# Kernel tuning notes

Measured on AMD Instinct MI355X. Metric: run time of the kernel, lower is better.

## Reference

```python
import jax, jax.numpy as jnp
import numpy as np

K = 3
KK = K * K
EPS = 1e-5


def conv2d(x, w, b, pad):
    y = jax.lax.conv_general_dilated(x, w, (1, 1), [(pad, pad), (pad, pad)],
                                     dimension_numbers=("NCHW", "OIHW", "NCHW"))
    return y + b[None, :, None, None]


def bn(x, g, b, m, v):
    inv = g / jnp.sqrt(v + EPS)
    return x * inv[None, :, None, None] + (b - m * inv)[None, :, None, None]


def deform_sample(x, dy, dx):
    # x: [B,C,H,W]; dy,dx: [B,KK,H,W] -> sampled [B,C,KK,H,W] (bilinear, zeros outside)
    B, C, H, W = x.shape
    k = jnp.arange(K, dtype=x.dtype) - 1.0  # pad=1, dilation=1, stride=1
    ky = jnp.repeat(k, K)  # [KK] row offsets
    kx = jnp.tile(k, K)    # [KK] col offsets
    hh = jnp.arange(H, dtype=x.dtype)
    ww = jnp.arange(W, dtype=x.dtype)
    py = hh[None, :, None] + ky[:, None, None] + dy  # [B,KK,H,W]
    px = ww[None, None, :] + kx[:, None, None] + dx

    def sample_one(img, py, px):
        y0f = jnp.floor(py); x0f = jnp.floor(px)
        wy = py - y0f; wx = px - x0f
        y0 = y0f.astype(jnp.int32); x0 = x0f.astype(jnp.int32)

        def gather(yi, xi, w):
            valid = (yi >= 0) & (yi < H) & (xi >= 0) & (xi < W)
            yc = jnp.clip(yi, 0, H - 1); xc = jnp.clip(xi, 0, W - 1)
            v = img[:, yc, xc]  # [C,KK,H,W]
            return v * (w * valid)[None]

        return (gather(y0, x0, (1 - wy) * (1 - wx)) +
                gather(y0, x0 + 1, (1 - wy) * wx) +
                gather(y0 + 1, x0, wy * (1 - wx)) +
                gather(y0 + 1, x0 + 1, wy * wx))

    return jax.vmap(sample_one)(x, py, px)


def setup_inputs() -> dict:
    key = jax.random.key(0)
    ks = jax.random.split(key, 16)
    B, C, H, W = 8, 256, 64, 64
    d = {
        "feature": jax.random.normal(ks[0], (B, C, H, W), jnp.float32),
        "p1_w": jax.random.normal(ks[1], (C, C, 1, 1), jnp.float32) * 0.05,
        "p1_b": jax.random.normal(ks[2], (C,), jnp.float32) * 0.05,
        "bn1_g": jax.random.normal(ks[3], (C,), jnp.float32) * 0.1 + 1.0,
        "bn1_b": jax.random.normal(ks[4], (C,), jnp.float32) * 0.05,
        "bn1_m": jax.random.normal(ks[5], (C,), jnp.float32) * 0.05,
        "bn1_v": jax.random.uniform(ks[6], (C,), jnp.float32) + 0.5,
        "off_w": jax.random.normal(ks[7], (3 * KK, 2 * C, K, K), jnp.float32) * 0.01,
        "off_b": jax.random.normal(ks[8], (3 * KK,), jnp.float32) * 0.01,
        "dcn_w": jax.random.normal(ks[9], (C, C, K, K), jnp.float32) * 0.05,
        "dcn_b": jax.random.normal(ks[10], (C,), jnp.float32) * 0.05,
        "bn2_g": jax.random.normal(ks[11], (C,), jnp.float32) * 0.1 + 1.0,
        "bn2_b": jax.random.normal(ks[12], (C,), jnp.float32) * 0.05,
        "bn2_m": jax.random.normal(ks[13], (C,), jnp.float32) * 0.05,
        "bn2_v": jax.random.uniform(ks[14], (C,), jnp.float32) + 0.5,
    }
    return d


def reference(feature, p1_w, p1_b, bn1_g, bn1_b, bn1_m, bn1_v,
              off_w, off_b, dcn_w, dcn_b, bn2_g, bn2_b, bn2_m, bn2_v):
    flipped = feature[..., ::-1]                      # flip last (W) axis
    proj = bn(conv2d(feature, p1_w, p1_b, 0), bn1_g, bn1_b, bn1_m, bn1_v)
    # DCNv2: offsets/mask from concat(flipped, proj)
    concat = jnp.concatenate([flipped, proj], axis=1)
    off = conv2d(concat, off_w, off_b, 1)             # [B,27,H,W]
    dy = off[:, :KK]
    dx = off[:, KK:2 * KK]
    mask = jax.nn.sigmoid(off[:, 2 * KK:])            # [B,KK,H,W]
    sampled = deform_sample(flipped, dy, dx)          # [B,C,KK,H,W]
    O = dcn_w.shape[0]
    y = jnp.einsum("bckhw,ock->bohw", sampled * mask[:, None], dcn_w.reshape(O, -1, KK))
    y = y + dcn_b[None, :, None, None]
    y = bn(y, bn2_g, bn2_b, bn2_m, bn2_v)
    return jax.nn.relu(proj + y)
```

## Files before the change

### kernel.cpp

```cpp
#include <hip/hip_runtime.h>
#include <hip/hip_bf16.h>
#include <math.h>

typedef __attribute__((ext_vector_type(8))) short short8;
typedef __attribute__((ext_vector_type(4))) short short4v;
typedef __attribute__((ext_vector_type(4))) float f32x4;
typedef __attribute__((ext_vector_type(2))) float f32x2;

__device__ __forceinline__ float bs2f(short s){
    union { unsigned u; float f; } x; x.u = ((unsigned)(unsigned short)s) << 16; return x.f;
}
__device__ __forceinline__ short f2bs(float f){
    union { float f; unsigned u; } x; x.f = f;
    unsigned r = x.u + 0x7fff + ((x.u >> 16) & 1);
    return (short)(r >> 16);
}
__device__ __forceinline__ f32x2 up2(unsigned u){
    union { unsigned u; float f; } lo, hi;
    lo.u = u << 16; hi.u = u & 0xffff0000u;
    f32x2 r; r.x = lo.f; r.y = hi.f; return r;
}
__device__ __forceinline__ unsigned pk2rn(float lo, float hi){
    __hip_bfloat162 h = __float22bfloat162_rn(make_float2(lo, hi));
    union { __hip_bfloat162 h; unsigned u; } cv; cv.h = h; return cv.u;
}
__device__ __forceinline__ void gl2lds16(const void* g, void* l){
    __builtin_amdgcn_global_load_lds(
        (const __attribute__((address_space(1))) void*)g,
        (__attribute__((address_space(3))) void*)l, 16, 0, 0);
}
__device__ __forceinline__ void hard_barrier(){
    __builtin_amdgcn_sched_barrier(0);
    __builtin_amdgcn_s_barrier();
    __builtin_amdgcn_sched_barrier(0);
}
__device__ __forceinline__ void lds_barrier(){
    __builtin_amdgcn_sched_barrier(0);
    asm volatile("s_waitcnt lgkmcnt(0)" ::: "memory");
    __builtin_amdgcn_s_barrier();
    __builtin_amdgcn_sched_barrier(0);
}

#define XPB ((size_t)66*66*512)


__global__ void k_prep(const float* __restrict__ p1_w, const float* __restrict__ p1_b,
                       const float* __restrict__ bn1_g, const float* __restrict__ bn1_b,
                       const float* __restrict__ bn1_m, const float* __restrict__ bn1_v,
                       const float* __restrict__ off_w,
                       const float* __restrict__ dcn_w, const float* __restrict__ dcn_b,
                       const float* __restrict__ bn2_g, const float* __restrict__ bn2_b,
                       const float* __restrict__ bn2_m, const float* __restrict__ bn2_v,
                       short* __restrict__ p1_wb, short* __restrict__ Wofrag,
                       short* __restrict__ Wfrag,
                       float* __restrict__ bias1f, float* __restrict__ inv2f,
                       float* __restrict__ bias2f, unsigned* __restrict__ XpadU)
{
    int blk = blockIdx.x, t = threadIdx.x;
    if (blk == 0) {
        float inv1 = bn1_g[t] / sqrtf(bn1_v[t] + 1e-5f);
        bias1f[t] = p1_b[t] * inv1 + bn1_b[t] - bn1_m[t] * inv1;
        float inv2 = bn2_g[t] / sqrtf(bn2_v[t] + 1e-5f);
        inv2f[t] = inv2;
        bias2f[t] = dcn_b[t] * inv2 + bn2_b[t] - bn2_m[t] * inv2;
    } else if (blk <= 256) {
        int o = blk - 1;
        float inv1 = bn1_g[o] / sqrtf(bn1_v[o] + 1e-5f);
        p1_wb[o*256 + t] = f2bs(p1_w[o*256 + t] * inv1);
    } else if (blk <= 512) {
        int o = blk - 257;
        const float* src = dcn_w + (size_t)o*2304;
        uint4* dst = (uint4*)Wfrag;
        int strip = o >> 4, lnn = o & 15;
        #pragma unroll
        for (int r = 0; r < 2; ++r) {
            int j = r*256 + t;
            if (j < 288) {
                int tap = j >> 5, c0 = (j & 31) * 8;
                union { short s[8]; uint4 u; } v;
                #pragma unroll
                for (int e = 0; e < 8; ++e)
                    v.s[e] = f2bs(src[(c0 + e)*9 + tap]);
                dst[(size_t)((j >> 2)*16 + strip)*64 + (j & 3)*16 + lnn] = v.u;
            }
        }
    } else if (blk <= 584) {
        int gidx = (blk - 513)*256 + t;
        int kc = gidx >> 7;
        int rem = gidx & 127;
        int strip = rem >> 6, lane2 = rem & 63;
        int ln2 = lane2 & 15, q2 = lane2 >> 4;
        int row = strip*16 + ln2;
        union { short s[8]; uint4 u; } v;
        #pragma unroll
        for (int e = 0; e < 8; ++e) {
            int k = kc*32 + q2*8 + e;
            int tap = k >> 9, ci = k & 511;
            v.s[e] = (row < 27) ? f2bs(off_w[(size_t)row*4608 + ci*9 + tap]) : (short)0;
        }
        ((uint4*)Wofrag)[gidx] = v.u;
    } else {
        int hb = blk - 585;
        int b = hb / 260, i = hb % 260;
        int y, x;
        if (i < 66)       { y = 0;  x = i; }
        else if (i < 132) { y = 65; x = i - 66; }
        else { int j = i - 132; y = 1 + (j >> 1); x = (j & 1) * 65; }
        XpadU[((size_t)(b*66 + y)*66 + x)*256 + t] = 0u;
    }
}

__global__ __launch_bounds__(512, 2) void k_fproj(
    const float* __restrict__ feature, short* Xpad,
    const short* __restrict__ p1_wb, const float* __restrict__ bias1f)
{
    __shared__ __align__(16) unsigned char sh_u[16640];
    __shared__ __align__(16) short Bt[8][2048];
    float (*tile)[65] = (float(*)[65])sh_u;
    short* Ash = (short*)sh_u;
    int bid = blockIdx.x;
    int b = bid & 7, h = bid >> 3;
    int t = threadIdx.x;
    int lane = t & 63, w = t >> 6;
    int lw = t & 63, li = t >> 6;
    int ln = lane & 15, q = lane >> 4;
    int r16 = lane >> 2;
    int sq  = (lane & 3) ^ ((lane >> 3) & 3);
    int rq  = (q ^ ((ln >> 1) & 3)) * 8;
    size_t rowbase = (size_t)(b*66 + h + 1)*66;

    for (int cg = 0; cg < 4; ++cg) {
        int c0 = cg * 64;
        #pragma unroll
        for (int j = 0; j < 8; ++j) {
            int cl = j*8 + li;
            tile[cl][63 - lw] = feature[((b*256 + c0 + cl)*64 + h)*64 + lw];
        }
        __syncthreads();
        #pragma unroll
        for (int j = 0; j < 8; ++j) {
            int x = j*8 + li;
            short s  = f2bs(tile[lw][x]);
            Xpad[(rowbase + x + 1)*512 + c0 + lw] = s;
            short sB = f2bs(tile[lw][63 - x]);
            int c = c0 + lw;
            int kt = c >> 5, kk = c & 31, p = kk >> 3, e = kk & 7;
            Bt[kt][x*32 + ((p ^ ((x >> 1) & 3)) << 3) + e] = sB;
        }
        __syncthreads();
    }

    f32x4 acc[2][4] = {};
    for (int kt = 0; kt < 8; ++kt) {
        int kcol = kt*32 + sq*8;
        #pragma unroll
        for (int i = 0; i < 2; ++i) {
            int row = w*32 + i*16 + r16;
            gl2lds16(p1_wb + (size_t)row*256 + kcol, Ash + (w*32 + i*16)*32);
        }
        __syncthreads();
        short8 af[2], bfr[4];
        #pragma unroll
        for (int i = 0; i < 2; ++i)
            af[i] = *(const short8*)&Ash[(w*32 + i*16 + ln)*32 + rq];
        #pragma unroll
        for (int j = 0; j < 4; ++j)
            bfr[j] = *(const short8*)&Bt[kt][(j*16 + ln)*32 + rq];
        #pragma unroll
        for (int i = 0; i < 2; ++i)
            #pragma unroll
            for (int j = 0; j < 4; ++j)
                acc[i][j] = __builtin_amdgcn_mfma_f32_16x16x32_bf16(af[i], bfr[j], acc[i][j], 0, 0, 0);
        __syncthreads();
    }
    #pragma unroll
    for (int i = 0; i < 2; ++i) {
        int ob = w*32 + i*16 + q*4;
        #pragma unroll
        for (int j = 0; j < 4; ++j) {
            int x = j*16 + ln;
            size_t xb = (rowbase + x + 1)*512 + 256 + ob;
            short4v st;
            st.x = f2bs(acc[i][j][0] + bias1f[ob]);
            st.y = f2bs(acc[i][j][1] + bias1f[ob+1]);
            st.z = f2bs(acc[i][j][2] + bias1f[ob+2]);
            st.w = f2bs(acc[i][j][3] + bias1f[ob+3]);
            *(short4v*)&Xpad[xb] = st;
        }
    }
}

#define ALOAD4(kn_, A_)                                                   \
    A_##0 = Wf4[(size_t)(((kn_)*2+0)*16 + tw0)*64 + lane];                \
    A_##1 = Wf4[(size_t)(((kn_)*2+0)*16 + tw1)*64 + lane];                \
    A_##2 = Wf4[(size_t)(((kn_)*2+1)*16 + tw0)*64 + lane];                \
    A_##3 = Wf4[(size_t)(((kn_)*2+1)*16 + tw1)*64 + lane];

#define MMPHASE(A_)                                                       \
    {                                                                     \
        short8 af00 = *(short8*)&A_##0, af01 = *(short8*)&A_##1;          \
        short8 af10 = *(short8*)&A_##2, af11 = *(short8*)&A_##3;          \
        short8 bfr;                                                       \
        _Pragma("unroll")                                                 \
        for (int jj = 0; jj < 4; ++jj) {                                  \
            bfr = *(const short8*)&Bsh[0][(jj*16 + ln)*32 + rq];          \
            acc[0][jj] = __builtin_amdgcn_mfma_f32_16x16x32_bf16(af00, bfr, acc[0][jj], 0, 0, 0); \
            acc[1][jj] = __builtin_amdgcn_mfma_f32_16x16x32_bf16(af01, bfr, acc[1][jj], 0, 0, 0); \
        }                                                                 \
        _Pragma("unroll")                                                 \
        for (int jj = 0; jj < 4; ++jj) {                                  \
            bfr = *(const short8*)&Bsh[1][(jj*16 + ln)*32 + rq];          \
            acc[0][jj] = __builtin_amdgcn_mfma_f32_16x16x32_bf16(af10, bfr, acc[0][jj], 0, 0, 0); \
            acc[1][jj] = __builtin_amdgcn_mfma_f32_16x16x32_bf16(af11, bfr, acc[1][jj], 0, 0, 0); \
        }                                                                 \
    }

#define WINX(kc2_, AC_, AN_, UC_, VN_)                                    \
    {                                                                     \
        int kn_ = (kc2_) < 35 ? (kc2_) + 1 : 35;                          \
        ALOAD4(kn_, AN_);                                                 \
        GATHER(kn_, VN_);                                                 \
        __builtin_amdgcn_sched_barrier(0);                                \
        BLEND(UC_, (kc2_) >> 2);                                          \
        lds_barrier();                                                    \
        MMPHASE(AC_);                                                     \
        hard_barrier();                                                   \
    }

__global__ __launch_bounds__(512, 4) void k_gemm(
    const short* __restrict__ Xpad,
    const short* __restrict__ Wfrag,
    const uint4* __restrict__ Wof4,
    const float* __restrict__ off_b,
    const float* __restrict__ inv2f, const float* __restrict__ bias2f,
    float* __restrict__ out)
{
    __shared__ __align__(16) unsigned char shU[32768];
    __shared__ float red[27][65];
    short (*BshO)[2048] = (short(*)[2048])shU;
    short (*Bsh)[2048]  = (short(*)[2048])shU;
    unsigned* c_pk = (unsigned*)(shU + 8192);
    float*    c_w  = (float*)(shU + 10496);
    int bid = blockIdx.x;
    int b = bid & 7, h = bid >> 3;
    int t = threadIdx.x;
    int lane = t & 63, w = t >> 6;
    int ln = lane & 15, q = lane >> 4;
    int rq  = (q ^ ((ln >> 1) & 3)) * 8;
    int tw0 = w*2, tw1 = w*2 + 1;
    const uint4* Wf4 = (const uint4*)Wfrag;

    {
        int wr = w >> 2, wc = w & 3;
        int r16 = lane >> 2;
        int sq  = (lane & 3) ^ ((lane >> 3) & 3);
        const short* xb = Xpad + (size_t)b*XPB;
        f32x4 oacc = {};
        for (int it = 0; it < 18; ++it) {
            int tap = it >> 1;
            int dy = tap/3 - 1, dx = tap%3 - 1;
            uint4 a[8];
            #pragma unroll
            for (int s = 0; s < 8; ++s)
                a[s] = Wof4[(size_t)((it*8 + s)*2 + wr)*64 + lane];
            {
                int k = it*256 + w*32;
                #pragma unroll
                for (int g = 0; g < 4; ++g) {
                    int row = g*16 + r16;
                    const short* gB = xb + ((size_t)(h + 1 + dy)*66 + (row + dx + 1))*512
                                         + (k & 511) + sq*8;
                    gl2lds16(gB, &BshO[w][(g*16)*32]);
                }
            }
            __syncthreads();
            #pragma unroll
            for (int s = 0; s < 8; ++s) {
                short8 af  = *(short8*)&a[s];
                short8 bfr = *(const short8*)&BshO[s][(wc*16 + ln)*32 + rq];
                oacc = __builtin_amdgcn_mfma_f32_16x16x32_bf16(af, bfr, oacc, 0, 0, 0);
            }
            __syncthreads();
        }
        int x = wc*16 + ln;
        #pragma unroll
        for (int r = 0; r < 4; ++r) {
            int oc = wr*16 + q*4 + r;
            if (oc < 27)
                red[oc][x] = oacc[r] + off_b[oc];
        }
    }
    __syncthreads();

    for (int e = t; e < 576; e += 512) {
        int p = e / 9, k = e % 9;
        float dy = red[k][p];
        float dx = red[9+k][p];
        float ms = red[18+k][p];
        ms = 1.f / (1.f + expf(-ms));
        float py = (float)h + (float)(k/3 - 1) + dy;
        float px = (float)p + (float)(k%3 - 1) + dx;
        float y0f = floorf(py), x0f = floorf(px);
        float wy = py - y0f, wx = px - x0f;
        int y0 = (int)y0f, x0 = (int)x0f;
        int y1 = y0 + 1, x1 = x0 + 1;
        float vy0 = (y0 >= 0 && y0 < 64) ? 1.f : 0.f;
        float vy1 = (y1 >= 0 && y1 < 64) ? 1.f : 0.f;
        float vx0 = (x0 >= 0 && x0 < 64) ? 1.f : 0.f;
        float vx1 = (x1 >= 0 && x1 < 64) ? 1.f : 0.f;
        int y0c = min(max(y0,0),63), y1c = min(max(y1,0),63);
        int x0c = min(max(x0,0),63), x1c = min(max(x1,0),63);
        unsigned cell = (unsigned)(((y0c+1)*66 + x0c+1)*128);
        unsigned sx = (x1c != x0c) ? 1u : 0u;
        unsigned sy = (y1c != y0c) ? 1u : 0u;
        c_pk[e] = cell | (sx << 20) | (sy << 21);
        c_w[e*4+0] = ms * (1.f-wy)*(1.f-wx) * vy0*vx0;
        c_w[e*4+1] = ms * (1.f-wy)*wx       * vy0*vx1;
        c_w[e*4+2] = ms * wy*(1.f-wx)       * vy1*vx0;
        c_w[e*4+3] = ms * wy*wx             * vy1*vx1;
    }
    __syncthreads();

    const uint2* fT = (const uint2*)Xpad + (size_t)b*(XPB/4);
    int pr = t >> 3;
    int jo = t & 7;
    int pe9 = pr*9;
    short* bdst = &Bsh[jo >> 2][pr*32 + (((jo & 3) ^ ((pr >> 1) & 3)) << 3)];

    f32x4 acc[2][4] = {};
    uint4 U[4], V[4];
    uint4 a00, a01, a02, a03;
    uint4 a10, a11, a12, a13;

    auto GATHER = [&](int win, uint4 (&dst)[4]) {
        unsigned pw = c_pk[pe9 + (win >> 2)];
        int o00 = pw & 0xFFFFF;
        int dxs = (pw >> 13) & 128;
        int dys = ((pw >> 8) & 0x2000) | ((pw >> 13) & 0x100);
        int cin = ((win & 3) << 4) + jo*2;
        const uint2* p0 = fT + (o00 + cin);
        dst[0] = *(const uint4*)(p0);
        dst[1] = *(const uint4*)(p0 + dxs);
        dst[2] = *(const uint4*)(p0 + dys);
        dst[3] = *(const uint4*)(p0 + dys + dxs);
    };
    auto BLEND = [&](uint4 (&uc)[4], int tap) {
        const float4 cw = *(const float4*)&c_w[(pe9 + tap)*4];
        f32x2 Wx; Wx.x = cw.x; Wx.y = cw.x;
        f32x2 Wy; Wy.x = cw.y; Wy.y = cw.y;
        f32x2 Wz; Wz.x = cw.z; Wz.y = cw.z;
        f32x2 Ww; Ww.x = cw.w; Ww.y = cw.w;
        f32x2 G0 = Wx*up2(uc[0].x) + Wy*up2(uc[1].x) + Wz*up2(uc[2].x) + Ww*up2(uc[3].x);
        f32x2 G1 = Wx*up2(uc[0].y) + Wy*up2(uc[1].y) + Wz*up2(uc[2].y) + Ww*up2(uc[3].y);
        f32x2 G2 = Wx*up2(uc[0].z) + Wy*up2(uc[1].z) + Wz*up2(uc[2].z) + Ww*up2(uc[3].z);
        f32x2 G3 = Wx*up2(uc[0].w) + Wy*up2(uc[1].w) + Wz*up2(uc[2].w) + Ww*up2(uc[3].w);
        uint4 pkv;
        pkv.x = pk2rn(G0.x, G0.y);
        pkv.y = pk2rn(G1.x, G1.y);
        pkv.z = pk2rn(G2.x, G2.y);
        pkv.w = pk2rn(G3.x, G3.y);
        *(uint4*)bdst = pkv;
    };

    ALOAD4(0, a0);
    GATHER(0, U);
    __builtin_amdgcn_sched_barrier(0);
    #pragma unroll 1
    for (int kc2 = 0; kc2 < 36; kc2 += 2) {
        WINX(kc2,     a0, a1, U, V);
        WINX(kc2 + 1, a1, a0, V, U);
    }

    #pragma unroll
    for (int i = 0; i < 2; ++i) {
        int ob = w*32 + i*16 + q*4;
        #pragma unroll
        for (int jj = 0; jj < 4; ++jj) {
            int p = jj*16 + ln;
            size_t xb = ((size_t)(b*66 + h + 1)*66 + p + 1)*512 + 256 + ob;
            short4v prr = *(const short4v*)&Xpad[xb];
            #pragma unroll
            for (int r = 0; r < 4; ++r) {
                int o = ob + r;
                size_t idx = ((size_t)(b*256 + o))*4096 + h*64 + p;
                float rs = bs2f(((const short*)&prr)[r]);
                float v = rs + acc[i][jj][r]*inv2f[o] + bias2f[o];
                out[idx] = v < 0.f ? 0.f : v;
            }
        }
    }
}

extern "C" void kernel_launch(void* const* d_in, const int* in_sizes, int n_in,
                              void* d_out, int out_size, void* d_ws, size_t ws_size,
                              hipStream_t stream)
{
    const float* feature = (const float*)d_in[0];
    const float* p1_w  = (const float*)d_in[1];
    const float* p1_b  = (const float*)d_in[2];
    const float* bn1_g = (const float*)d_in[3];
    const float* bn1_b = (const float*)d_in[4];
    const float* bn1_m = (const float*)d_in[5];
    const float* bn1_v = (const float*)d_in[6];
    const float* off_w = (const float*)d_in[7];
    const float* off_b = (const float*)d_in[8];
    const float* dcn_w = (const float*)d_in[9];
    const float* dcn_b = (const float*)d_in[10];
    const float* bn2_g = (const float*)d_in[11];
    const float* bn2_b = (const float*)d_in[12];
    const float* bn2_m = (const float*)d_in[13];
    const float* bn2_v = (const float*)d_in[14];

    float* ws = (float*)d_ws;
    short* Xpad   = (short*)ws;
    short* p1_wb  = (short*)(ws + 9805824);
    short* Wofrag = (short*)(ws + 9838592);
    short* Wfrag  = (short*)(ws + 9912320);
    float* bias1f = ws + 10207232;
    float* inv2f  = ws + 10207488;
    float* bias2f = ws + 10207744;

    k_prep<<<2665, 256, 0, stream>>>(p1_w, p1_b, bn1_g, bn1_b, bn1_m, bn1_v,
                                     off_w, dcn_w, dcn_b, bn2_g, bn2_b, bn2_m, bn2_v,
                                     p1_wb, Wofrag, Wfrag, bias1f, inv2f, bias2f,
                                     (unsigned*)Xpad);
    k_fproj<<<512, 512, 0, stream>>>(feature, Xpad, p1_wb, bias1f);
    k_gemm<<<512, 512, 0, stream>>>(Xpad, Wfrag, (const uint4*)Wofrag, off_b,
                                    inv2f, bias2f, (float*)d_out);
}
```

Measured before the change: 214.8 us.

## Split GEMM output channels across two blocks and stage dcn weights in LDS

The deformable GEMM kernel now launches twice as many blocks. Each block computes 128 output channels for one (batch, row) instead of all 256, so each wave keeps one 16-channel strip and half the accumulators and A-fragment registers. The aim is more parallelism and lower register pressure, at the cost of duplicating the per-row offset computation and the bilinear gather/blend work in both halves. Separately, the weight prep kernel first loads each dcn_w row into shared memory with coalesced reads, then does the strided transposed reads from LDS.

```diff
diff --git a/kernel.cpp b/kernel.cpp
--- a/kernel.cpp
+++ b/kernel.cpp
@@ -56,6 +56,7 @@
                        float* __restrict__ bias1f, float* __restrict__ inv2f,
                        float* __restrict__ bias2f, unsigned* __restrict__ XpadU)
 {
+    __shared__ float s_stage[4608];
     int blk = blockIdx.x, t = threadIdx.x;
     if (blk == 0) {
         float inv1 = bn1_g[t] / sqrtf(bn1_v[t] + 1e-5f);
@@ -70,6 +71,8 @@
     } else if (blk <= 512) {
         int o = blk - 257;
         const float* src = dcn_w + (size_t)o*2304;
+        for (int j = t; j < 2304; j += 256) s_stage[j] = src[j];
+        __syncthreads();
         uint4* dst = (uint4*)Wfrag;
         int strip = o >> 4, lnn = o & 15;
         #pragma unroll
@@ -80,12 +83,13 @@
                 union { short s[8]; uint4 u; } v;
                 #pragma unroll
                 for (int e = 0; e < 8; ++e)
-                    v.s[e] = f2bs(src[(c0 + e)*9 + tap]);
+                    v.s[e] = f2bs(s_stage[(c0 + e)*9 + tap]);
                 dst[(size_t)((j >> 2)*16 + strip)*64 + (j & 3)*16 + lnn] = v.u;
             }
         }
     } else if (blk <= 584) {
-        int gidx = (blk - 513)*256 + t;
+        int bb = blk - 513;
+        int gidx = bb*256 + t;
         int kc = gidx >> 7;
         int rem = gidx & 127;
         int strip = rem >> 6, lane2 = rem & 63;
@@ -190,35 +194,30 @@
     }
 }
 
-#define ALOAD4(kn_, A_)                                                   \
-    A_##0 = Wf4[(size_t)(((kn_)*2+0)*16 + tw0)*64 + lane];                \
-    A_##1 = Wf4[(size_t)(((kn_)*2+0)*16 + tw1)*64 + lane];                \
-    A_##2 = Wf4[(size_t)(((kn_)*2+1)*16 + tw0)*64 + lane];                \
-    A_##3 = Wf4[(size_t)(((kn_)*2+1)*16 + tw1)*64 + lane];
+#define ALOAD2(kn_, A_)                                                   \
+    A_##0 = Wf4[(size_t)(((kn_)*2+0)*16 + st)*64 + lane];                 \
+    A_##1 = Wf4[(size_t)(((kn_)*2+1)*16 + st)*64 + lane];
 
 #define MMPHASE(A_)                                                       \
     {                                                                     \
-        short8 af00 = *(short8*)&A_##0, af01 = *(short8*)&A_##1;          \
-        short8 af10 = *(short8*)&A_##2, af11 = *(short8*)&A_##3;          \
+        short8 af0 = *(short8*)&A_##0, af1 = *(short8*)&A_##1;            \
         short8 bfr;                                                       \
         _Pragma("unroll")                                                 \
         for (int jj = 0; jj < 4; ++jj) {                                  \
             bfr = *(const short8*)&Bsh[0][(jj*16 + ln)*32 + rq];          \
-            acc[0][jj] = __builtin_amdgcn_mfma_f32_16x16x32_bf16(af00, bfr, acc[0][jj], 0, 0, 0); \
-            acc[1][jj] = __builtin_amdgcn_mfma_f32_16x16x32_bf16(af01, bfr, acc[1][jj], 0, 0, 0); \
+            acc[jj] = __builtin_amdgcn_mfma_f32_16x16x32_bf16(af0, bfr, acc[jj], 0, 0, 0); \
         }                                                                 \
         _Pragma("unroll")                                                 \
         for (int jj = 0; jj < 4; ++jj) {                                  \
             bfr = *(const short8*)&Bsh[1][(jj*16 + ln)*32 + rq];          \
-            acc[0][jj] = __builtin_amdgcn_mfma_f32_16x16x32_bf16(af10, bfr, acc[0][jj], 0, 0, 0); \
-            acc[1][jj] = __builtin_amdgcn_mfma_f32_16x16x32_bf16(af11, bfr, acc[1][jj], 0, 0, 0); \
+            acc[jj] = __builtin_amdgcn_mfma_f32_16x16x32_bf16(af1, bfr, acc[jj], 0, 0, 0); \
         }                                                                 \
     }
 
 #define WINX(kc2_, AC_, AN_, UC_, VN_)                                    \
     {                                                                     \
         int kn_ = (kc2_) < 35 ? (kc2_) + 1 : 35;                          \
-        ALOAD4(kn_, AN_);                                                 \
+        ALOAD2(kn_, AN_);                                                 \
         GATHER(kn_, VN_);                                                 \
         __builtin_amdgcn_sched_barrier(0);                                \
         BLEND(UC_, (kc2_) >> 2);                                          \
@@ -242,12 +241,12 @@
     unsigned* c_pk = (unsigned*)(shU + 8192);
     float*    c_w  = (float*)(shU + 10496);
     int bid = blockIdx.x;
-    int b = bid & 7, h = bid >> 3;
+    int b = bid & 7, mh = (bid >> 3) & 1, h = bid >> 4;
     int t = threadIdx.x;
     int lane = t & 63, w = t >> 6;
     int ln = lane & 15, q = lane >> 4;
     int rq  = (q ^ ((ln >> 1) & 3)) * 8;
-    int tw0 = w*2, tw1 = w*2 + 1;
+    int st = mh*8 + w;
     const uint4* Wf4 = (const uint4*)Wfrag;
 
     {
@@ -327,10 +326,10 @@
     int pe9 = pr*9;
     short* bdst = &Bsh[jo >> 2][pr*32 + (((jo & 3) ^ ((pr >> 1) & 3)) << 3)];
 
-    f32x4 acc[2][4] = {};
+    f32x4 acc[4] = {};
     uint4 U[4], V[4];
-    uint4 a00, a01, a02, a03;
-    uint4 a10, a11, a12, a13;
+    uint4 a00, a01;
+    uint4 a10, a11;
 
     auto GATHER = [&](int win, uint4 (&dst)[4]) {
         unsigned pw = c_pk[pe9 + (win >> 2)];
@@ -362,7 +361,7 @@
         *(uint4*)bdst = pkv;
     };
 
-    ALOAD4(0, a0);
+    ALOAD2(0, a0);
     GATHER(0, U);
     __builtin_amdgcn_sched_barrier(0);
     #pragma unroll 1
@@ -371,9 +370,8 @@
         WINX(kc2 + 1, a1, a0, V, U);
     }
 
-    #pragma unroll
-    for (int i = 0; i < 2; ++i) {
-        int ob = w*32 + i*16 + q*4;
+    {
+        int ob = st*16 + q*4;
         #pragma unroll
         for (int jj = 0; jj < 4; ++jj) {
             int p = jj*16 + ln;
@@ -384,7 +382,7 @@
                 int o = ob + r;
                 size_t idx = ((size_t)(b*256 + o))*4096 + h*64 + p;
                 float rs = bs2f(((const short*)&prr)[r]);
-                float v = rs + acc[i][jj][r]*inv2f[o] + bias2f[o];
+                float v = rs + acc[jj][r]*inv2f[o] + bias2f[o];
                 out[idx] = v < 0.f ? 0.f : v;
             }
         }
@@ -425,6 +423,6 @@
                                      p1_wb, Wofrag, Wfrag, bias1f, inv2f, bias2f,
                                      (unsigned*)Xpad);
     k_fproj<<<512, 512, 0, stream>>>(feature, Xpad, p1_wb, bias1f);
-    k_gemm<<<512, 512, 0, stream>>>(Xpad, Wfrag, (const uint4*)Wofrag, off_b,
-                                    inv2f, bias2f, (float*)d_out);
-}
+    k_gemm<<<1024, 512, 0, stream>>>(Xpad, Wfrag, (const uint4*)Wofrag, off_b,
+                                     inv2f, bias2f, (float*)d_out);
+}
```

Result: slower. 273.2 us (+27.2%).
